# Optimization experiments

Hardware: AMD Instinct MI355X
Metric: run time of the kernel (lower is better)

The kernel has to match this reference:

```python
import jax, jax.numpy as jnp
import numpy as np

K = 5            # trend_kernel_size
PAD = K // 2
EPS = 1e-5

def _ricker(k):
    # Ricker (mexican-hat) wavelet used as the Peaks kernel
    a = k / 4.0
    t = np.arange(k, dtype=np.float64) - (k - 1) / 2.0
    A = 2.0 / (np.sqrt(3.0 * a) * np.pi ** 0.25)
    return (A * (1.0 - (t / a) ** 2) * np.exp(-t ** 2 / (2.0 * a ** 2))).astype(np.float32)

def _ramp(k):
    # centered linear ramp -> local slope estimator for the Trend kernel
    return (np.linspace(-1.0, 1.0, k) / k).astype(np.float32)

_PEAK_W = jnp.asarray(_ricker(K))
_RAMP_W = jnp.asarray(_ramp(K))

def tconv(x, w):
    # 'same'-padded cross-correlation along the time axis (axis=2) of (B,C,T,H,W)
    T = x.shape[2]
    xp = jnp.pad(x, ((0, 0), (0, 0), (PAD, PAD), (0, 0), (0, 0)))
    out = w[0] * jax.lax.dynamic_slice_in_dim(xp, 0, T, axis=2)
    for j in range(1, K):
        out = out + w[j] * jax.lax.dynamic_slice_in_dim(xp, j, T, axis=2)
    return out

def bn(x, gamma, beta, axes):
    # training-mode batch norm over `axes`, channel axis = 1
    m = x.mean(axes, keepdims=True)
    v = x.var(axes, keepdims=True)
    xn = (x - m) * jax.lax.rsqrt(v + EPS)
    shp = [1] * x.ndim
    shp[1] = -1
    return xn * gamma.reshape(shp) + beta.reshape(shp)


def setup_inputs() -> dict:
    key = jax.random.key(0)
    ks = jax.random.split(key, 8)
    B, C, T, H, W = 4, 3, 12, 256, 256
    CH0 = 32
    return {
        'x':      jax.random.normal(ks[0], (B, C, T, H, W), jnp.float32),
        'w0':     jax.random.normal(ks[1], (CH0, C), jnp.float32) * 0.1,
        'g0':     jnp.ones((CH0,), jnp.float32),
        'b0':     jnp.zeros((CH0,), jnp.float32),
        'wrt':    jax.random.normal(ks[2], (1, CH0), jnp.float32) * 0.1,
        'grt':    jnp.ones((1,), jnp.float32),
        'brt':    jnp.zeros((1,), jnp.float32),
        'wtt':    jax.random.normal(ks[3], (1, C), jnp.float32) * 0.1,
        'gtt':    jnp.ones((1,), jnp.float32),
        'btt':    jnp.zeros((1,), jnp.float32),
        'w_th':   jax.random.normal(ks[4], (CH0, T), jnp.float32) * 0.1,
        'b_th':   jnp.zeros((CH0,), jnp.float32),
        'g_min':  jnp.ones((CH0,), jnp.float32),
        'b_min':  jnp.zeros((CH0,), jnp.float32),
        'g_max':  jnp.ones((CH0,), jnp.float32),
        'b_max':  jnp.zeros((CH0,), jnp.float32),
        'g_mean': jnp.ones((CH0,), jnp.float32),
        'b_mean': jnp.zeros((CH0,), jnp.float32),
    }


def reference(x, w0, g0, b0, wrt, grt, brt, wtt, gtt, btt,
              w_th, b_th, g_min, b_min, g_max, b_max, g_mean, b_mean):
    act = jax.nn.silu
    # --- per-band temporal kernels (vectorized over all bands/pixels) ---
    peak = tconv(x, _PEAK_W)                       # Peaks: ricker wavelet
    slope = tconv(x, _RAMP_W)                      # Trend: local slope
    trend = peak + jax.nn.relu(slope) + jax.nn.relu(-slope)  # (B,C,T,H,W)
    # --- time_conv0: 1x1x1 conv3d + BN3d + act ---
    h = act(bn(jnp.einsum('bcthw,oc->bothw', x, w0), g0, b0, (0, 2, 3, 4)))  # (B,32,T,H,W)
    # --- reduce_to_time / reduce_trend_to_time: 1x1x1 conv3d to 1 channel ---
    rt = act(bn(jnp.einsum('bcthw,oc->bothw', h, wrt), grt, brt, (0, 2, 3, 4)))[:, 0]      # (B,T,H,W)
    tt = act(bn(jnp.einsum('bcthw,oc->bothw', trend, wtt), gtt, btt, (0, 2, 3, 4)))[:, 0]  # (B,T,H,W)
    # --- time_to_hidden: 1x1 conv2d over the time-as-channels axis ---
    time_logits = jnp.einsum('bthw,ot->bohw', rt + tt, w_th) + b_th[None, :, None, None]
    # --- channel reductions over time + BN2d + act (mean branch uses max, as in source) ---
    xmin = h.min(axis=2)
    xmax = h.max(axis=2)
    cmin = act(bn(xmin, g_min, b_min, (0, 2, 3)))
    cmax = act(bn(xmax, g_max, b_max, (0, 2, 3)))
    cmean = act(bn(xmax, g_mean, b_mean, (0, 2, 3)))
    enc = time_logits + cmin + cmax + cmean        # (B,32,H,W)
    # --- InstanceNorm2d(affine=False) ---
    m = enc.mean((2, 3), keepdims=True)
    v = enc.var((2, 3), keepdims=True)
    return (enc - m) * jax.lax.rsqrt(v + EPS)
```

## Files before the change

### kernel.cpp

```cpp
#include <hip/hip_runtime.h>
#include <math.h>

#define HW_    65536
#define THW_   786432
#define NP     262144
#define N1_    3145728.0
#define N3_    262144.0

__device__ __constant__ float PW_[5] = {-0.33647654f, 0.20279402f, 0.77575913f, 0.20279402f, -0.33647654f};
__device__ __constant__ float RW_[5] = {-0.2f, -0.1f, 0.0f, 0.1f, 0.2f};

typedef __fp16 fp16x2 __attribute__((ext_vector_type(2)));
union H2U { fp16x2 h; unsigned int u; };
__device__ __forceinline__ unsigned int packh(float a, float b) {
  H2U x; x.h = __builtin_amdgcn_cvt_pkrtz(a, b); return x.u;
}
__device__ __forceinline__ float2 unpackh(unsigned int v) {
  H2U x; x.u = v; return make_float2((float)x.h.x, (float)x.h.y);
}

__device__ __forceinline__ float wred64(float v) {
#pragma unroll
  for (int m = 32; m > 0; m >>= 1) v += __shfl_xor(v, m, 64);
  return v;
}

__device__ __forceinline__ float fsilu(float y) {
  float e = __expf(-y);
  return y * __builtin_amdgcn_rcpf(1.0f + e);
}


__global__ void k_init(double* dws) {
  int i = blockIdx.x * 256 + threadIdx.x;
  if (i < 416) dws[i] = 0.0;
}

__global__ __launch_bounds__(256) void k_xstats(const float* __restrict__ x, double* __restrict__ dws) {
  const int v = blockIdx.x * 256 + threadIdx.x;
  const float4* x4 = (const float4*)x;
  float s0 = 0, s1 = 0, s2 = 0, p00 = 0, p01 = 0, p02 = 0, p11 = 0, p12 = 0, p22 = 0;
#pragma unroll
  for (int b = 0; b < 4; b++) {
    float4 a0 = x4[(size_t)(b * 3 + 0) * 196608 + v];
    float4 a1 = x4[(size_t)(b * 3 + 1) * 196608 + v];
    float4 a2 = x4[(size_t)(b * 3 + 2) * 196608 + v];
    s0 += a0.x + a0.y + a0.z + a0.w;
    s1 += a1.x + a1.y + a1.z + a1.w;
    s2 += a2.x + a2.y + a2.z + a2.w;
    p00 += a0.x * a0.x + a0.y * a0.y + a0.z * a0.z + a0.w * a0.w;
    p11 += a1.x * a1.x + a1.y * a1.y + a1.z * a1.z + a1.w * a1.w;
    p22 += a2.x * a2.x + a2.y * a2.y + a2.z * a2.z + a2.w * a2.w;
    p01 += a0.x * a1.x + a0.y * a1.y + a0.z * a1.z + a0.w * a1.w;
    p02 += a0.x * a2.x + a0.y * a2.y + a0.z * a2.z + a0.w * a2.w;
    p12 += a1.x * a2.x + a1.y * a2.y + a1.z * a2.z + a1.w * a2.w;
  }
  float vals[9] = {s0, s1, s2, p00, p01, p02, p11, p12, p22};
  __shared__ float red[4][9];
  int wave = threadIdx.x >> 6, lane = threadIdx.x & 63;
#pragma unroll
  for (int q = 0; q < 9; q++) vals[q] = wred64(vals[q]);
  if (lane == 0) {
#pragma unroll
    for (int q = 0; q < 9; q++) red[wave][q] = vals[q];
  }
  __syncthreads();
  if (threadIdx.x < 9) {
    double t = (double)red[0][threadIdx.x] + red[1][threadIdx.x] + red[2][threadIdx.x] + red[3][threadIdx.x];
    atomicAdd(&dws[threadIdx.x], t);
  }
}

__global__ void k_fin0(const double* __restrict__ dws, const float* __restrict__ w0,
                       const float* __restrict__ g0, const float* __restrict__ b0, float* __restrict__ cf) {
  int o = threadIdx.x;
  if (o >= 32) return;
  double mu0 = dws[0] / N1_, mu1 = dws[1] / N1_, mu2 = dws[2] / N1_;
  double M00 = dws[3] / N1_, M01 = dws[4] / N1_, M02 = dws[5] / N1_;
  double M11 = dws[6] / N1_, M12 = dws[7] / N1_, M22 = dws[8] / N1_;
  double c0 = w0[o * 3 + 0], c1 = w0[o * 3 + 1], c2 = w0[o * 3 + 2];
  double Ey = c0 * mu0 + c1 * mu1 + c2 * mu2;
  double Ey2 = c0 * c0 * M00 + c1 * c1 * M11 + c2 * c2 * M22 +
               2.0 * (c0 * c1 * M01 + c0 * c2 * M02 + c1 * c2 * M12);
  double var = Ey2 - Ey * Ey;
  double alpha = (double)g0[o] / sqrt(var + 1e-5);
  cf[o * 3 + 0] = (float)(alpha * c0);
  cf[o * 3 + 1] = (float)(alpha * c1);
  cf[o * 3 + 2] = (float)(alpha * c2);
  cf[96 + o] = (float)((double)b0[o] - Ey * alpha);
}

__global__ __launch_bounds__(256) void k_passB(const float* __restrict__ x, const float* __restrict__ wrt,
                                               const float* __restrict__ wtt, const float* __restrict__ cf,
                                               unsigned int* __restrict__ pRT, unsigned int* __restrict__ pMM) {
  const int pix = blockIdx.x * 256 + threadIdx.x;
  const int b = pix >> 16, hw = pix & 65535;
  const float* xp = x + (size_t)b * 3 * THW_ + hw;
  float xv[3][12];
#pragma unroll
  for (int c = 0; c < 3; c++)
#pragma unroll
    for (int t = 0; t < 12; t++) xv[c][t] = xp[(size_t)(c * 12 + t) * HW_];
  float wt[3] = {wtt[0], wtt[1], wtt[2]};
  float ttp[12];
#pragma unroll
  for (int t = 0; t < 12; t++) {
    float acc = 0.f;
#pragma unroll
    for (int c = 0; c < 3; c++) {
      float pk = 0.f, sl = 0.f;
#pragma unroll
      for (int j = 0; j < 5; j++) {
        int tj = t - 2 + j;
        if (tj >= 0 && tj < 12) {
          pk = fmaf(PW_[j], xv[c][tj], pk);
          sl = fmaf(RW_[j], xv[c][tj], sl);
        }
      }
      acc = fmaf(wt[c], pk + fabsf(sl), acc);
    }
    ttp[t] = acc;
  }
  float rt_t[12];
#pragma unroll
  for (int t = 0; t < 12; t++) rt_t[t] = 0.f;
#pragma unroll
  for (int o = 0; o < 32; o++) {
    float a0 = cf[o * 3], a1 = cf[o * 3 + 1], a2 = cf[o * 3 + 2];
    float bet = cf[96 + o], wo = wrt[o];
    float mn = 3.4e38f, mx = -3.4e38f;
#pragma unroll
    for (int t = 0; t < 12; t++) {
      float y = fmaf(a0, xv[0][t], fmaf(a1, xv[1][t], fmaf(a2, xv[2][t], bet)));
      float h = fsilu(y);
      mn = fminf(mn, h);
      mx = fmaxf(mx, h);
      rt_t[t] = fmaf(wo, h, rt_t[t]);
    }
    pMM[o * NP + pix] = packh(mn, mx);
  }
#pragma unroll
  for (int t = 0; t < 12; t++) pRT[t * NP + pix] = packh(rt_t[t], ttp[t]);
}

__global__ __launch_bounds__(256) void k_stats(const unsigned int* __restrict__ pRT,
                                               const unsigned int* __restrict__ pMM,
                                               double* __restrict__ dws) {
  __shared__ float red[4][4];
  int bid = blockIdx.x, tid = threadIdx.x;
  float s0 = 0, s1 = 0, s2 = 0, s3 = 0;
  if (bid < 96) {
    const uint4* p = (const uint4*)pRT;
    int base = bid * 256 + tid;
#pragma unroll 4
    for (int it = 0; it < 32; it++) {
      uint4 v = p[base + it * 24576];
      float2 a = unpackh(v.x), b = unpackh(v.y), c = unpackh(v.z), d = unpackh(v.w);
      s0 += a.x + b.x + c.x + d.x;
      s1 += a.x * a.x + b.x * b.x + c.x * c.x + d.x * d.x;
      s2 += a.y + b.y + c.y + d.y;
      s3 += a.y * a.y + b.y * b.y + c.y * c.y + d.y * d.y;
    }
  } else {
    int o = (bid - 96) >> 3, sub = (bid - 96) & 7;
    const uint4* p = (const uint4*)(pMM + (size_t)o * NP);
    int base = sub * 256 + tid;
#pragma unroll 4
    for (int it = 0; it < 32; it++) {
      uint4 v = p[base + it * 2048];
      float2 a = unpackh(v.x), b = unpackh(v.y), c = unpackh(v.z), d = unpackh(v.w);
      s0 += a.x + b.x + c.x + d.x;
      s1 += a.x * a.x + b.x * b.x + c.x * c.x + d.x * d.x;
      s2 += a.y + b.y + c.y + d.y;
      s3 += a.y * a.y + b.y * b.y + c.y * c.y + d.y * d.y;
    }
  }
  s0 = wred64(s0); s1 = wred64(s1); s2 = wred64(s2); s3 = wred64(s3);
  int wave = tid >> 6, lane = tid & 63;
  if (lane == 0) { red[wave][0] = s0; red[wave][1] = s1; red[wave][2] = s2; red[wave][3] = s3; }
  __syncthreads();
  if (tid < 4) {
    double v = (double)red[0][tid] + red[1][tid] + red[2][tid] + red[3][tid];
    if (bid < 96) atomicAdd(&dws[9 + tid], v);
    else { int o = (bid - 96) >> 3; atomicAdd(&dws[16 + tid * 32 + o], v); }
  }
}

__global__ void k_finB(const double* __restrict__ dws, const float* __restrict__ grt, const float* __restrict__ brt,
                       const float* __restrict__ gtt, const float* __restrict__ btt, const float* __restrict__ gmin,
                       const float* __restrict__ bmin, const float* __restrict__ gmax, const float* __restrict__ bmax,
                       const float* __restrict__ gmean, const float* __restrict__ bmean, float* __restrict__ cf) {
  int tid = threadIdx.x;
  if (tid == 32) {
    double m = dws[9] / N1_, v = dws[10] / N1_ - m * m;
    double a = (double)grt[0] / sqrt(v + 1e-5);
    cf[128] = (float)a;
    cf[129] = (float)((double)brt[0] - m * a);
    m = dws[11] / N1_;
    v = dws[12] / N1_ - m * m;
    a = (double)gtt[0] / sqrt(v + 1e-5);
    cf[130] = (float)a;
    cf[131] = (float)((double)btt[0] - m * a);
  }
  if (tid < 32) {
    double m = dws[16 + tid] / N3_, v = dws[48 + tid] / N3_ - m * m;
    double a = (double)gmin[tid] / sqrt(v + 1e-5);
    cf[132 + tid] = (float)a;
    cf[164 + tid] = (float)((double)bmin[tid] - m * a);
    double mm = dws[80 + tid] / N3_, vv = dws[112 + tid] / N3_ - mm * mm;
    a = (double)gmax[tid] / sqrt(vv + 1e-5);
    cf[196 + tid] = (float)a;
    cf[228 + tid] = (float)((double)bmax[tid] - mm * a);
    a = (double)gmean[tid] / sqrt(vv + 1e-5);
    cf[260 + tid] = (float)a;
    cf[292 + tid] = (float)((double)bmean[tid] - mm * a);
  }
}

__global__ __launch_bounds__(256) void k_passC(const unsigned int* __restrict__ pRT,
                                               const unsigned int* __restrict__ pMM,
                                               const float* __restrict__ wth, const float* __restrict__ bth,
                                               const float* __restrict__ cf, float* __restrict__ out) {
  const int pix = blockIdx.x * 256 + threadIdx.x;
  const int b = pix >> 16, hw = pix & 65535;
  float art = cf[128], brt_ = cf[129], att = cf[130], btt_ = cf[131];
  float rtt[12];
#pragma unroll
  for (int t = 0; t < 12; t++) {
    float2 v = unpackh(pRT[t * NP + pix]);
    rtt[t] = fsilu(fmaf(art, v.x, brt_)) + fsilu(fmaf(att, v.y, btt_));
  }
  float* po = out + (size_t)b * 32 * HW_ + hw;
#pragma unroll
  for (int o = 0; o < 32; o++) {
    float2 mm = unpackh(pMM[o * NP + pix]);
    float tl = bth[o];
#pragma unroll
    for (int t = 0; t < 12; t++) tl = fmaf(wth[o * 12 + t], rtt[t], tl);
    float e = tl + fsilu(fmaf(cf[132 + o], mm.x, cf[164 + o]))
                 + fsilu(fmaf(cf[196 + o], mm.y, cf[228 + o]))
                 + fsilu(fmaf(cf[260 + o], mm.y, cf[292 + o]));
    po[(size_t)o * HW_] = e;
  }
}

__global__ __launch_bounds__(256) void k_encstats(const float* __restrict__ out, double* __restrict__ dws) {
  __shared__ float red[4][2];
  int s = blockIdx.x >> 2, sub = blockIdx.x & 3, tid = threadIdx.x;
  const float4* p = (const float4*)(out + ((size_t)s << 16));
  float S = 0, SS = 0;
#pragma unroll 4
  for (int it = 0; it < 16; it++) {
    float4 a = p[sub * 256 + tid + it * 1024];
    S += a.x + a.y + a.z + a.w;
    SS += a.x * a.x + a.y * a.y + a.z * a.z + a.w * a.w;
  }
  S = wred64(S); SS = wred64(SS);
  int wave = tid >> 6, lane = tid & 63;
  if (lane == 0) { red[wave][0] = S; red[wave][1] = SS; }
  __syncthreads();
  if (tid < 2) {
    double v = (double)red[0][tid] + red[1][tid] + red[2][tid] + red[3][tid];
    atomicAdd(&dws[160 + 2 * s + tid], v);
  }
}

__global__ __launch_bounds__(256) void k_inorm(const double* __restrict__ dws, float* __restrict__ out) {
  int s = blockIdx.y;
  double S = dws[160 + s * 2], SS = dws[161 + s * 2];
  double m = S / 65536.0, v = SS / 65536.0 - m * m;
  float rstd = (float)(1.0 / sqrt(v + 1e-5));
  float mf = (float)m;
  float4* p = (float4*)(out + ((size_t)s << 16));
  int i = blockIdx.x * 256 + threadIdx.x;
  float4 a = p[i];
  a.x = (a.x - mf) * rstd;
  a.y = (a.y - mf) * rstd;
  a.z = (a.z - mf) * rstd;
  a.w = (a.w - mf) * rstd;
  p[i] = a;
}

extern "C" void kernel_launch(void* const* d_in, const int* in_sizes, int n_in,
                              void* d_out, int out_size, void* d_ws, size_t ws_size,
                              hipStream_t stream) {
  const float* x     = (const float*)d_in[0];
  const float* w0    = (const float*)d_in[1];
  const float* g0    = (const float*)d_in[2];
  const float* b0    = (const float*)d_in[3];
  const float* wrt   = (const float*)d_in[4];
  const float* grt   = (const float*)d_in[5];
  const float* brt   = (const float*)d_in[6];
  const float* wtt   = (const float*)d_in[7];
  const float* gtt   = (const float*)d_in[8];
  const float* btt   = (const float*)d_in[9];
  const float* wth   = (const float*)d_in[10];
  const float* bth   = (const float*)d_in[11];
  const float* gmin  = (const float*)d_in[12];
  const float* bmin  = (const float*)d_in[13];
  const float* gmax  = (const float*)d_in[14];
  const float* bmax  = (const float*)d_in[15];
  const float* gmean = (const float*)d_in[16];
  const float* bmean = (const float*)d_in[17];
  double* dws = (double*)d_ws;
  float* cf = (float*)((char*)d_ws + 4096);
  unsigned int* pRT = (unsigned int*)((char*)d_ws + 8192);
  unsigned int* pMM = pRT + 12 * NP;
  float* out = (float*)d_out;

  hipLaunchKernelGGL(k_init, dim3(2), dim3(256), 0, stream, dws);
  hipLaunchKernelGGL(k_xstats, dim3(768), dim3(256), 0, stream, x, dws);
  hipLaunchKernelGGL(k_fin0, dim3(1), dim3(32), 0, stream, dws, w0, g0, b0, cf);
  hipLaunchKernelGGL(k_passB, dim3(1024), dim3(256), 0, stream, x, wrt, wtt, cf, pRT, pMM);
  hipLaunchKernelGGL(k_stats, dim3(352), dim3(256), 0, stream, pRT, pMM, dws);
  hipLaunchKernelGGL(k_finB, dim3(1), dim3(64), 0, stream, dws, grt, brt, gtt, btt,
                     gmin, bmin, gmax, bmax, gmean, bmean, cf);
  hipLaunchKernelGGL(k_passC, dim3(1024), dim3(256), 0, stream, pRT, pMM, wth, bth, cf, out);
  hipLaunchKernelGGL(k_encstats, dim3(512), dim3(256), 0, stream, out, dws);
  hipLaunchKernelGGL(k_inorm, dim3(64, 128), dim3(256), 0, stream, dws, out);
}
```

Measured before the change: 125.2 us.

## Fuse BN statistics into producer kernels with sharded double atomics

Folds the separate k_stats and k_encstats reduction kernels into k_passB and k_passC. Each block reduces its own values through LDS tiles and warp shuffles and atomically adds partial sums into 8-way or 4-way sharded double slots, which the finalize kernels then sum. This drops two launches and the re-read of the fp16 intermediates and the output from global memory. In exchange it adds LDS usage (about 33 KB per block) that may lower occupancy, plus many more atomics, and statistics now come from unrounded fp32 values rather than the fp16-packed ones.

```diff
diff --git a/kernel.cpp b/kernel.cpp
--- a/kernel.cpp
+++ b/kernel.cpp
@@ -7,6 +7,11 @@
 #define N1_    3145728.0
 #define N3_    262144.0
 
+#define XB 0
+#define SB 72
+#define EB 1128
+#define DWN 2152
+
 __device__ __constant__ float PW_[5] = {-0.33647654f, 0.20279402f, 0.77575913f, 0.20279402f, -0.33647654f};
 __device__ __constant__ float RW_[5] = {-0.2f, -0.1f, 0.0f, 0.1f, 0.2f};
 
@@ -30,10 +35,9 @@
   return y * __builtin_amdgcn_rcpf(1.0f + e);
 }
 
-
 __global__ void k_init(double* dws) {
   int i = blockIdx.x * 256 + threadIdx.x;
-  if (i < 416) dws[i] = 0.0;
+  if (i < DWN) dws[i] = 0.0;
 }
 
 __global__ __launch_bounds__(256) void k_xstats(const float* __restrict__ x, double* __restrict__ dws) {
@@ -67,7 +71,7 @@
   __syncthreads();
   if (threadIdx.x < 9) {
     double t = (double)red[0][threadIdx.x] + red[1][threadIdx.x] + red[2][threadIdx.x] + red[3][threadIdx.x];
-    atomicAdd(&dws[threadIdx.x], t);
+    atomicAdd(&dws[XB + threadIdx.x * 8 + (blockIdx.x & 7)], t);
   }
 }
 
@@ -75,9 +79,16 @@
                        const float* __restrict__ g0, const float* __restrict__ b0, float* __restrict__ cf) {
   int o = threadIdx.x;
   if (o >= 32) return;
-  double mu0 = dws[0] / N1_, mu1 = dws[1] / N1_, mu2 = dws[2] / N1_;
-  double M00 = dws[3] / N1_, M01 = dws[4] / N1_, M02 = dws[5] / N1_;
-  double M11 = dws[6] / N1_, M12 = dws[7] / N1_, M22 = dws[8] / N1_;
+  double q[9];
+#pragma unroll
+  for (int i = 0; i < 9; i++) {
+    double t = 0;
+#pragma unroll
+    for (int s = 0; s < 8; s++) t += dws[XB + i * 8 + s];
+    q[i] = t / N1_;
+  }
+  double mu0 = q[0], mu1 = q[1], mu2 = q[2];
+  double M00 = q[3], M01 = q[4], M02 = q[5], M11 = q[6], M12 = q[7], M22 = q[8];
   double c0 = w0[o * 3 + 0], c1 = w0[o * 3 + 1], c2 = w0[o * 3 + 2];
   double Ey = c0 * mu0 + c1 * mu1 + c2 * mu2;
   double Ey2 = c0 * c0 * M00 + c1 * c1 * M11 + c2 * c2 * M22 +
@@ -92,9 +103,13 @@
 
 __global__ __launch_bounds__(256) void k_passB(const float* __restrict__ x, const float* __restrict__ wrt,
                                                const float* __restrict__ wtt, const float* __restrict__ cf,
-                                               unsigned int* __restrict__ pRT, unsigned int* __restrict__ pMM) {
-  const int pix = blockIdx.x * 256 + threadIdx.x;
+                                               unsigned int* __restrict__ pRT, unsigned int* __restrict__ pMM,
+                                               double* __restrict__ dws) {
+  const int tid = threadIdx.x;
+  const int pix = blockIdx.x * 256 + tid;
   const int b = pix >> 16, hw = pix & 65535;
+  __shared__ unsigned int lmm[32 * 264];
+  __shared__ float red[4][4];
   const float* xp = x + (size_t)b * 3 * THW_ + hw;
   float xv[3][12];
 #pragma unroll
@@ -137,52 +152,52 @@
       mx = fmaxf(mx, h);
       rt_t[t] = fmaf(wo, h, rt_t[t]);
     }
-    pMM[o * NP + pix] = packh(mn, mx);
+    unsigned int pk = packh(mn, mx);
+    pMM[o * NP + pix] = pk;
+    lmm[o * 264 + tid] = pk;
   }
 #pragma unroll
   for (int t = 0; t < 12; t++) pRT[t * NP + pix] = packh(rt_t[t], ttp[t]);
-}
-
-__global__ __launch_bounds__(256) void k_stats(const unsigned int* __restrict__ pRT,
-                                               const unsigned int* __restrict__ pMM,
-                                               double* __restrict__ dws) {
-  __shared__ float red[4][4];
-  int bid = blockIdx.x, tid = threadIdx.x;
-  float s0 = 0, s1 = 0, s2 = 0, s3 = 0;
-  if (bid < 96) {
-    const uint4* p = (const uint4*)pRT;
-    int base = bid * 256 + tid;
-#pragma unroll 4
-    for (int it = 0; it < 32; it++) {
-      uint4 v = p[base + it * 24576];
-      float2 a = unpackh(v.x), b = unpackh(v.y), c = unpackh(v.z), d = unpackh(v.w);
-      s0 += a.x + b.x + c.x + d.x;
-      s1 += a.x * a.x + b.x * b.x + c.x * c.x + d.x * d.x;
-      s2 += a.y + b.y + c.y + d.y;
-      s3 += a.y * a.y + b.y * b.y + c.y * c.y + d.y * d.y;
-    }
-  } else {
-    int o = (bid - 96) >> 3, sub = (bid - 96) & 7;
-    const uint4* p = (const uint4*)(pMM + (size_t)o * NP);
-    int base = sub * 256 + tid;
-#pragma unroll 4
-    for (int it = 0; it < 32; it++) {
-      uint4 v = p[base + it * 2048];
-      float2 a = unpackh(v.x), b = unpackh(v.y), c = unpackh(v.z), d = unpackh(v.w);
-      s0 += a.x + b.x + c.x + d.x;
-      s1 += a.x * a.x + b.x * b.x + c.x * c.x + d.x * d.x;
-      s2 += a.y + b.y + c.y + d.y;
-      s3 += a.y * a.y + b.y * b.y + c.y * c.y + d.y * d.y;
-    }
-  }
-  s0 = wred64(s0); s1 = wred64(s1); s2 = wred64(s2); s3 = wred64(s3);
-  int wave = tid >> 6, lane = tid & 63;
-  if (lane == 0) { red[wave][0] = s0; red[wave][1] = s1; red[wave][2] = s2; red[wave][3] = s3; }
+
+  {
+    float srt = 0.f, ssrt = 0.f, stt = 0.f, sstt = 0.f;
+#pragma unroll
+    for (int t = 0; t < 12; t++) {
+      srt += rt_t[t];  ssrt = fmaf(rt_t[t], rt_t[t], ssrt);
+      stt += ttp[t];   sstt = fmaf(ttp[t], ttp[t], sstt);
+    }
+    srt = wred64(srt); ssrt = wred64(ssrt); stt = wred64(stt); sstt = wred64(sstt);
+    int wave = tid >> 6, lane = tid & 63;
+    if (lane == 0) { red[wave][0] = srt; red[wave][1] = ssrt; red[wave][2] = stt; red[wave][3] = sstt; }
+  }
   __syncthreads();
   if (tid < 4) {
     double v = (double)red[0][tid] + red[1][tid] + red[2][tid] + red[3][tid];
-    if (bid < 96) atomicAdd(&dws[9 + tid], v);
-    else { int o = (bid - 96) >> 3; atomicAdd(&dws[16 + tid * 32 + o], v); }
+    atomicAdd(&dws[SB + (128 + tid) * 8 + (blockIdx.x & 7)], v);
+  }
+  {
+    int o = tid >> 3, j = tid & 7;
+    float smn = 0, smn2 = 0, smx = 0, smx2 = 0;
+#pragma unroll
+    for (int k = 0; k < 32; k++) {
+      float2 mm = unpackh(lmm[o * 264 + j + k * 8]);
+      smn += mm.x; smn2 = fmaf(mm.x, mm.x, smn2);
+      smx += mm.y; smx2 = fmaf(mm.y, mm.y, smx2);
+    }
+#pragma unroll
+    for (int m = 1; m < 8; m <<= 1) {
+      smn  += __shfl_xor(smn, m, 64);
+      smn2 += __shfl_xor(smn2, m, 64);
+      smx  += __shfl_xor(smx, m, 64);
+      smx2 += __shfl_xor(smx2, m, 64);
+    }
+    if (j == 0) {
+      int sh = blockIdx.x & 7;
+      atomicAdd(&dws[SB + (o * 4 + 0) * 8 + sh], (double)smn);
+      atomicAdd(&dws[SB + (o * 4 + 1) * 8 + sh], (double)smn2);
+      atomicAdd(&dws[SB + (o * 4 + 2) * 8 + sh], (double)smx);
+      atomicAdd(&dws[SB + (o * 4 + 3) * 8 + sh], (double)smx2);
+    }
   }
 }
 
@@ -192,22 +207,37 @@
                        const float* __restrict__ gmean, const float* __restrict__ bmean, float* __restrict__ cf) {
   int tid = threadIdx.x;
   if (tid == 32) {
-    double m = dws[9] / N1_, v = dws[10] / N1_ - m * m;
+    double q[4];
+#pragma unroll
+    for (int i = 0; i < 4; i++) {
+      double t = 0;
+#pragma unroll
+      for (int s = 0; s < 8; s++) t += dws[SB + (128 + i) * 8 + s];
+      q[i] = t / N1_;
+    }
+    double m = q[0], v = q[1] - m * m;
     double a = (double)grt[0] / sqrt(v + 1e-5);
     cf[128] = (float)a;
     cf[129] = (float)((double)brt[0] - m * a);
-    m = dws[11] / N1_;
-    v = dws[12] / N1_ - m * m;
+    m = q[2]; v = q[3] - m * m;
     a = (double)gtt[0] / sqrt(v + 1e-5);
     cf[130] = (float)a;
     cf[131] = (float)((double)btt[0] - m * a);
   }
   if (tid < 32) {
-    double m = dws[16 + tid] / N3_, v = dws[48 + tid] / N3_ - m * m;
+    double q[4];
+#pragma unroll
+    for (int i = 0; i < 4; i++) {
+      double t = 0;
+#pragma unroll
+      for (int s = 0; s < 8; s++) t += dws[SB + (tid * 4 + i) * 8 + s];
+      q[i] = t / N3_;
+    }
+    double m = q[0], v = q[1] - m * m;
     double a = (double)gmin[tid] / sqrt(v + 1e-5);
     cf[132 + tid] = (float)a;
     cf[164 + tid] = (float)((double)bmin[tid] - m * a);
-    double mm = dws[80 + tid] / N3_, vv = dws[112 + tid] / N3_ - mm * mm;
+    double mm = q[2], vv = q[3] - mm * mm;
     a = (double)gmax[tid] / sqrt(vv + 1e-5);
     cf[196 + tid] = (float)a;
     cf[228 + tid] = (float)((double)bmax[tid] - mm * a);
@@ -220,9 +250,12 @@
 __global__ __launch_bounds__(256) void k_passC(const unsigned int* __restrict__ pRT,
                                                const unsigned int* __restrict__ pMM,
                                                const float* __restrict__ wth, const float* __restrict__ bth,
-                                               const float* __restrict__ cf, float* __restrict__ out) {
-  const int pix = blockIdx.x * 256 + threadIdx.x;
+                                               const float* __restrict__ cf, float* __restrict__ out,
+                                               double* __restrict__ dws) {
+  const int tid = threadIdx.x;
+  const int pix = blockIdx.x * 256 + tid;
   const int b = pix >> 16, hw = pix & 65535;
+  __shared__ float lenc[32 * 264];
   float art = cf[128], brt_ = cf[129], att = cf[130], btt_ = cf[131];
   float rtt[12];
 #pragma unroll
@@ -241,33 +274,38 @@
                  + fsilu(fmaf(cf[196 + o], mm.y, cf[228 + o]))
                  + fsilu(fmaf(cf[260 + o], mm.y, cf[292 + o]));
     po[(size_t)o * HW_] = e;
-  }
-}
-
-__global__ __launch_bounds__(256) void k_encstats(const float* __restrict__ out, double* __restrict__ dws) {
-  __shared__ float red[4][2];
-  int s = blockIdx.x >> 2, sub = blockIdx.x & 3, tid = threadIdx.x;
-  const float4* p = (const float4*)(out + ((size_t)s << 16));
-  float S = 0, SS = 0;
-#pragma unroll 4
-  for (int it = 0; it < 16; it++) {
-    float4 a = p[sub * 256 + tid + it * 1024];
-    S += a.x + a.y + a.z + a.w;
-    SS += a.x * a.x + a.y * a.y + a.z * a.z + a.w * a.w;
-  }
-  S = wred64(S); SS = wred64(SS);
-  int wave = tid >> 6, lane = tid & 63;
-  if (lane == 0) { red[wave][0] = S; red[wave][1] = SS; }
+    lenc[o * 264 + tid] = e;
+  }
   __syncthreads();
-  if (tid < 2) {
-    double v = (double)red[0][tid] + red[1][tid] + red[2][tid] + red[3][tid];
-    atomicAdd(&dws[160 + 2 * s + tid], v);
+  {
+    int o = tid >> 3, j = tid & 7;
+    float s = 0, s2 = 0;
+#pragma unroll
+    for (int k = 0; k < 32; k++) {
+      float e = lenc[o * 264 + j + k * 8];
+      s += e; s2 = fmaf(e, e, s2);
+    }
+#pragma unroll
+    for (int m = 1; m < 8; m <<= 1) {
+      s  += __shfl_xor(s, m, 64);
+      s2 += __shfl_xor(s2, m, 64);
+    }
+    if (j == 0) {
+      int sh = blockIdx.x & 3;
+      atomicAdd(&dws[EB + ((b * 32 + o) * 2 + 0) * 4 + sh], (double)s);
+      atomicAdd(&dws[EB + ((b * 32 + o) * 2 + 1) * 4 + sh], (double)s2);
+    }
   }
 }
 
 __global__ __launch_bounds__(256) void k_inorm(const double* __restrict__ dws, float* __restrict__ out) {
   int s = blockIdx.y;
-  double S = dws[160 + s * 2], SS = dws[161 + s * 2];
+  double S = 0, SS = 0;
+#pragma unroll
+  for (int sh = 0; sh < 4; sh++) {
+    S  += dws[EB + (s * 2 + 0) * 4 + sh];
+    SS += dws[EB + (s * 2 + 1) * 4 + sh];
+  }
   double m = S / 65536.0, v = SS / 65536.0 - m * m;
   float rstd = (float)(1.0 / sqrt(v + 1e-5));
   float mf = (float)m;
@@ -303,19 +341,17 @@
   const float* gmean = (const float*)d_in[16];
   const float* bmean = (const float*)d_in[17];
   double* dws = (double*)d_ws;
-  float* cf = (float*)((char*)d_ws + 4096);
-  unsigned int* pRT = (unsigned int*)((char*)d_ws + 8192);
+  float* cf = (float*)((char*)d_ws + 32768);
+  unsigned int* pRT = (unsigned int*)((char*)d_ws + 65536);
   unsigned int* pMM = pRT + 12 * NP;
   float* out = (float*)d_out;
 
-  hipLaunchKernelGGL(k_init, dim3(2), dim3(256), 0, stream, dws);
+  hipLaunchKernelGGL(k_init, dim3(9), dim3(256), 0, stream, dws);
   hipLaunchKernelGGL(k_xstats, dim3(768), dim3(256), 0, stream, x, dws);
   hipLaunchKernelGGL(k_fin0, dim3(1), dim3(32), 0, stream, dws, w0, g0, b0, cf);
-  hipLaunchKernelGGL(k_passB, dim3(1024), dim3(256), 0, stream, x, wrt, wtt, cf, pRT, pMM);
-  hipLaunchKernelGGL(k_stats, dim3(352), dim3(256), 0, stream, pRT, pMM, dws);
+  hipLaunchKernelGGL(k_passB, dim3(1024), dim3(256), 0, stream, x, wrt, wtt, cf, pRT, pMM, dws);
   hipLaunchKernelGGL(k_finB, dim3(1), dim3(64), 0, stream, dws, grt, brt, gtt, btt,
                      gmin, bmin, gmax, bmax, gmean, bmean, cf);
-  hipLaunchKernelGGL(k_passC, dim3(1024), dim3(256), 0, stream, pRT, pMM, wth, bth, cf, out);
-  hipLaunchKernelGGL(k_encstats, dim3(512), dim3(256), 0, stream, out, dws);
+  hipLaunchKernelGGL(k_passC, dim3(1024), dim3(256), 0, stream, pRT, pMM, wth, bth, cf, out, dws);
   hipLaunchKernelGGL(k_inorm, dim3(64, 128), dim3(256), 0, stream, dws, out);
 }
```

Measured after the change: 145.9 us. 1.17x slower.
